# Performance work log

Hardware: AMD Instinct MI355X
Metric: run time of the kernel (lower is better)

The kernel has to match this reference:

```python
import jax, jax.numpy as jnp
import numpy as np

N_EMBD = 768
HIDDEN = 4 * N_EMBD
N_EXPERTS = 8
TOP_K = 2


def setup_inputs() -> dict:
    key = jax.random.key(0)
    ks = jax.random.split(key, 4)
    B, T, C, E, H = 4, 2048, N_EMBD, N_EXPERTS, HIDDEN
    x = jax.random.normal(ks[0], (B, T, C), dtype=jnp.float32)
    gate_w = jax.random.normal(ks[1], (E, C), dtype=jnp.float32) * 0.02
    gate_b = jnp.zeros((E,), dtype=jnp.float32)
    w_fc = jax.random.normal(ks[2], (E, H, C), dtype=jnp.float32) * 0.02
    b_fc = jnp.zeros((E, H), dtype=jnp.float32)
    w_proj = jax.random.normal(ks[3], (E, C, H), dtype=jnp.float32) * 0.02
    b_proj = jnp.zeros((E, C), dtype=jnp.float32)
    return {"x": x, "gate_w": gate_w, "gate_b": gate_b, "w_fc": w_fc,
            "b_fc": b_fc, "w_proj": w_proj, "b_proj": b_proj}


def reference(x, gate_w, gate_b, w_fc, b_fc, w_proj, b_proj):
    B, T, C = x.shape
    E = gate_b.shape[0]
    xf = x.reshape(-1, C)  # [N, C]
    # gating: Linear(C -> E), top-k, softmax over the k selected scores
    scores = xf @ gate_w.T + gate_b                      # [N, E]
    top_s, top_i = jax.lax.top_k(scores, TOP_K)          # [N, K]
    gates = jax.nn.softmax(top_s, axis=-1)               # [N, K]
    # combine weight per (token, expert): sum_k gate[t,k] * 1[top_i[t,k]==e]
    comb = jnp.sum(jax.nn.one_hot(top_i, E, dtype=xf.dtype) * gates[..., None], axis=1)  # [N, E]
    out = jnp.zeros_like(xf)
    for j in range(E):  # loop over fixed small expert count
        h = jax.nn.gelu(xf @ w_fc[j].T + b_fc[j], approximate=True)  # [N, H]
        y = h @ w_proj[j].T + b_proj[j]                              # [N, C]
        out = out + comb[:, j:j + 1] * y
    return out.reshape(B, T, C)
```

## Files before the change

### kernel.cpp

```cpp
#include <hip/hip_runtime.h>
#include <cmath>

#define N_TOK 8192
#define C_DIM 768
#define H_DIM 3072
#define NEXP  8
#define PADCAP 17408
#define MAXMT  136

typedef short short8 __attribute__((ext_vector_type(8)));
typedef float f32x4  __attribute__((ext_vector_type(4)));

__device__ __forceinline__ unsigned short f2b(float f) {
  unsigned int u = __float_as_uint(f);
  u += 0x7fffu + ((u >> 16) & 1u);
  return (unsigned short)(u >> 16);
}
__device__ __forceinline__ float b2f(unsigned short u) {
  return __uint_as_float((unsigned int)u << 16);
}
__device__ __forceinline__ void gll(const char* g, char* l) {
  __builtin_amdgcn_global_load_lds((const __attribute__((address_space(1))) void*)g,
                                   (__attribute__((address_space(3))) void*)l, 16, 0, 0);
}

__global__ __launch_bounds__(256) void gate_kernel(
    const float* __restrict__ x, const float* __restrict__ gw,
    const float* __restrict__ gb, int* __restrict__ counts,
    int* __restrict__ tok_e, int* __restrict__ tok_r, float* __restrict__ tok_w) {
  __shared__ float gwl[NEXP * C_DIM];
  __shared__ double red[256][NEXP];
  int tid = threadIdx.x;
  const float4* gw4 = (const float4*)gw;
  float4* gl4 = (float4*)gwl;
  for (int i = tid; i < NEXP * C_DIM / 4; i += 256) gl4[i] = gw4[i];
  __syncthreads();
  int tl = tid & 63;
  int kc = tid >> 6;
  int t = blockIdx.x * 64 + tl;
  double acc[NEXP];
#pragma unroll
  for (int e = 0; e < NEXP; e++) acc[e] = 0.0;
  const float* xr = x + (size_t)t * C_DIM;
  for (int k = kc * 192; k < kc * 192 + 192; k++) {
    double xv = (double)xr[k];
#pragma unroll
    for (int e = 0; e < NEXP; e++) acc[e] += xv * (double)gwl[e * C_DIM + k];
  }
#pragma unroll
  for (int e = 0; e < NEXP; e++) red[tid][e] = acc[e];
  __syncthreads();
  if (tid < 64) {
    double s[NEXP];
#pragma unroll
    for (int e = 0; e < NEXP; e++)
      s[e] = (double)gb[e] + red[tid][e] + red[tid + 64][e] + red[tid + 128][e] + red[tid + 192][e];
    double best = s[0], sec = -1e300; int bi = 0, si = -1;
#pragma unroll
    for (int e = 1; e < NEXP; e++) {
      if (s[e] > best)      { sec = best; si = bi; best = s[e]; bi = e; }
      else if (s[e] > sec)  { sec = s[e]; si = e; }
    }
    double ex = exp(sec - best);
    double den = 1.0 + ex;
    tok_e[2 * t] = bi;  tok_e[2 * t + 1] = si;
    tok_w[2 * t] = (float)(1.0 / den);  tok_w[2 * t + 1] = (float)(ex / den);
    tok_r[2 * t]     = atomicAdd(&counts[bi], 1);
    tok_r[2 * t + 1] = atomicAdd(&counts[si], 1);
  }
}

__global__ void offsets_kernel(const int* __restrict__ counts, int* __restrict__ po) {
  if (threadIdx.x == 0 && blockIdx.x == 0) {
    int s = 0;
    for (int e = 0; e < NEXP; e++) { po[e] = s; s += (counts[e] + 127) & ~127; }
    po[NEXP] = s;
  }
}

__global__ __launch_bounds__(256) void scatter_kernel(
    const int* __restrict__ tok_e, const int* __restrict__ tok_r,
    const float* __restrict__ tok_w, const int* __restrict__ po,
    int* __restrict__ perm_t, float* __restrict__ perm_w,
    int* __restrict__ tok_pos) {
  int t = blockIdx.x * 256 + threadIdx.x;
#pragma unroll
  for (int k = 0; k < 2; k++) {
    int e = tok_e[2 * t + k];
    int pos = po[e] + tok_r[2 * t + k];
    perm_t[pos] = t;
    perm_w[pos] = tok_w[2 * t + k];
    tok_pos[2 * t + k] = pos;
  }
}

__global__ __launch_bounds__(256) void gather_kernel(
    const float* __restrict__ x, const int* __restrict__ po,
    const int* __restrict__ perm_t, unsigned short* __restrict__ xg) {
  int row = blockIdx.x * 4 + (threadIdx.x >> 6);
  if (row >= po[NEXP]) return;
  int l = threadIdx.x & 63;
  int t = perm_t[row];
  const float4* src = (const float4*)(x + (size_t)t * C_DIM);
  ushort4* dst = (ushort4*)(xg + (size_t)row * C_DIM);
#pragma unroll
  for (int j = 0; j < 3; j++) {
    float4 v = src[l + j * 64];
    ushort4 o; o.x = f2b(v.x); o.y = f2b(v.y); o.z = f2b(v.z); o.w = f2b(v.w);
    dst[l + j * 64] = o;
  }
}

__global__ __launch_bounds__(256) void wconv_kernel(
    const float* __restrict__ wfc, const float* __restrict__ wproj,
    unsigned short* __restrict__ wfcb, unsigned short* __restrict__ wpjb) {
  const int n4 = NEXP * H_DIM * C_DIM / 4;
  int stride = gridDim.x * blockDim.x;
  for (int i = blockIdx.x * blockDim.x + threadIdx.x; i < 2 * n4; i += stride) {
    const float4* s; ushort4* d; int j;
    if (i < n4) { s = (const float4*)wfc;   d = (ushort4*)wfcb; j = i; }
    else        { s = (const float4*)wproj; d = (ushort4*)wpjb; j = i - n4; }
    float4 v = s[j];
    ushort4 o; o.x = f2b(v.x); o.y = f2b(v.y); o.z = f2b(v.z); o.w = f2b(v.w);
    d[j] = o;
  }
}

__device__ __forceinline__ void gemm_core512(
    const unsigned short* A, int lda, const unsigned short* B, int ldb, int K,
    char* lds, int tid, f32x4 acc[4][2]) {
  const int w = tid >> 6, l = tid & 63;
  const int wr = w >> 2, wc = w & 3;
  const int rowa = wr * 64 + (l & 15);
  const int rowb = wc * 32 + (l & 15);
  const int kc = l >> 4;
  const int sa0 = (kc ^ ((rowa >> 1) & 7)) * 16;
  const int sb0 = (kc ^ ((rowb >> 1) & 7)) * 16;
  const int r0 = tid >> 3,          cg0 = (tid & 7) ^ ((r0 >> 1) & 7);
  const int r1 = (512 + tid) >> 3,  cg1 = ((512 + tid) & 7) ^ ((r1 >> 1) & 7);
  const char* gA0 = (const char*)(A + (size_t)r0 * lda) + cg0 * 16;
  const char* gA1 = (const char*)(A + (size_t)r1 * lda) + cg1 * 16;
  const char* gB0 = (const char*)(B + (size_t)r0 * ldb) + cg0 * 16;
  const char* gB1 = (const char*)(B + (size_t)r1 * ldb) + cg1 * 16;
  const int wb = w * 1024;
  const int iters = K >> 6;
  gll(gA0, lds + wb);
  gll(gA1, lds + 8192 + wb);
  gll(gB0, lds + 16384 + wb);
  gll(gB1, lds + 24576 + wb);
#pragma unroll 1
  for (int kt = 0; kt < iters; kt++) {
    __syncthreads();
    if (kt + 1 < iters) {
      size_t kb = (size_t)(kt + 1) * 128;
      char* nb = lds + ((kt + 1) & 1) * 32768;
      gll(gA0 + kb, nb + wb);
      gll(gA1 + kb, nb + 8192 + wb);
      gll(gB0 + kb, nb + 16384 + wb);
      gll(gB1 + kb, nb + 24576 + wb);
    }
    char* bb = lds + (kt & 1) * 32768;
#pragma unroll
    for (int s = 0; s < 2; s++) {
      const int sxa = sa0 ^ (s << 6);
      const int sxb = sb0 ^ (s << 6);
      short8 af[4], bf2[2];
#pragma unroll
      for (int mi = 0; mi < 4; mi++)
        af[mi] = *(const short8*)(bb + (rowa + mi * 16) * 128 + sxa);
#pragma unroll
      for (int ni = 0; ni < 2; ni++)
        bf2[ni] = *(const short8*)(bb + 16384 + (rowb + ni * 16) * 128 + sxb);
#pragma unroll
      for (int mi = 0; mi < 4; mi++)
#pragma unroll
        for (int ni = 0; ni < 2; ni++)
          acc[mi][ni] = __builtin_amdgcn_mfma_f32_16x16x32_bf16(af[mi], bf2[ni], acc[mi][ni], 0, 0, 0);
    }
  }
}

__global__ __launch_bounds__(512, 4) void fc1_kernel(
    const unsigned short* __restrict__ xg, const unsigned short* __restrict__ wfcb,
    const float* __restrict__ bfc, const int* __restrict__ po,
    unsigned short* __restrict__ h) {
  __shared__ char lds[65536];
  int bid = blockIdx.x;
  int r8 = bid & 7, g8 = bid >> 3;
  int col = g8 % 24;
  int Sp  = g8 / 24;
  int y   = r8 * 17 + Sp;
  int row0 = y * 128;
  if (row0 >= po[NEXP]) return;
  int e = 0;
#pragma unroll
  for (int i = 1; i < NEXP; i++) if (row0 >= po[i]) e = i;
  int n0 = col * 128;
  int tid = threadIdx.x;
  f32x4 acc[4][2];
#pragma unroll
  for (int mi = 0; mi < 4; mi++)
#pragma unroll
    for (int ni = 0; ni < 2; ni++) acc[mi][ni] = (f32x4){0.f, 0.f, 0.f, 0.f};
  gemm_core512(xg + (size_t)row0 * C_DIM, C_DIM,
               wfcb + (size_t)e * H_DIM * C_DIM + (size_t)n0 * C_DIM, C_DIM, C_DIM,
               lds, tid, acc);
  int w = tid >> 6, l = tid & 63;
  int wr = w >> 2, wc = w & 3, q = l >> 4;
  const float* bias = bfc + (size_t)e * H_DIM;
#pragma unroll
  for (int ni = 0; ni < 2; ni++) {
    int colw = n0 + wc * 32 + ni * 16 + (l & 15);
    float bv = bias[colw];
#pragma unroll
    for (int mi = 0; mi < 4; mi++) {
#pragma unroll
      for (int r = 0; r < 4; r++) {
        int row = row0 + wr * 64 + mi * 16 + q * 4 + r;
        float v = acc[mi][ni][r] + bv;
        float z = v * fmaf(0.0356774081f, v * v, 0.7978845608f);
        float ex = __builtin_amdgcn_exp2f(-2.8853900818f * z);
        float g = v * __builtin_amdgcn_rcpf(1.0f + ex);
        h[(size_t)row * H_DIM + colw] = f2b(g);
      }
    }
  }
}

__global__ __launch_bounds__(512, 4) void fc2_kernel(
    const unsigned short* __restrict__ h, const unsigned short* __restrict__ wpjb,
    const float* __restrict__ bproj, const int* __restrict__ po,
    const float* __restrict__ perm_w, unsigned short* __restrict__ part) {
  __shared__ char lds[65536];
  int bid = blockIdx.x;
  int r8 = bid & 7, g8 = bid >> 3;
  int col = g8 % 6;
  int Sp  = g8 / 6;
  int S   = r8 * 34 + Sp;
  int z   = S / 136;
  int y   = S - z * 136;
  int row0 = y * 128;
  if (row0 >= po[NEXP]) return;
  int e = 0;
#pragma unroll
  for (int i = 1; i < NEXP; i++) if (row0 >= po[i]) e = i;
  int n0 = col * 128;
  int koff = z * (H_DIM / 2);
  int tid = threadIdx.x;
  f32x4 acc[4][2];
#pragma unroll
  for (int mi = 0; mi < 4; mi++)
#pragma unroll
    for (int ni = 0; ni < 2; ni++) acc[mi][ni] = (f32x4){0.f, 0.f, 0.f, 0.f};
  gemm_core512(h + (size_t)row0 * H_DIM + koff, H_DIM,
               wpjb + (size_t)e * C_DIM * H_DIM + (size_t)n0 * H_DIM + koff, H_DIM, H_DIM / 2,
               lds, tid, acc);
  int w = tid >> 6, l = tid & 63;
  int wr = w >> 2, wc = w & 3, q = l >> 4;
  const float* bias = bproj + (size_t)e * C_DIM;
  unsigned short* pz = part + (size_t)z * PADCAP * C_DIM;
#pragma unroll
  for (int mi = 0; mi < 4; mi++) {
#pragma unroll
    for (int r = 0; r < 4; r++) {
      int pos = row0 + wr * 64 + mi * 16 + q * 4 + r;
      float wgt = perm_w[pos];
#pragma unroll
      for (int ni = 0; ni < 2; ni++) {
        int colw = n0 + wc * 32 + ni * 16 + (l & 15);
        float v = acc[mi][ni][r];
        if (z == 0) v += bias[colw];
        pz[(size_t)pos * C_DIM + colw] = f2b(v * wgt);
      }
    }
  }
}

__global__ __launch_bounds__(256) void combine_kernel(
    const unsigned short* __restrict__ part, const int* __restrict__ tok_pos,
    float* __restrict__ out) {
  const int NC4 = C_DIM / 4;
  int idx = blockIdx.x * 256 + threadIdx.x;
  int t = idx / NC4, c4 = idx - t * NC4;
  int p0 = tok_pos[2 * t], p1 = tok_pos[2 * t + 1];
  const size_t SP = (size_t)PADCAP * C_DIM;
  const unsigned short* r00 = part + (size_t)p0 * C_DIM + c4 * 4;
  const unsigned short* r10 = part + (size_t)p1 * C_DIM + c4 * 4;
  ushort4 v00 = *(const ushort4*)r00;
  ushort4 v01 = *(const ushort4*)(r00 + SP);
  ushort4 v10 = *(const ushort4*)r10;
  ushort4 v11 = *(const ushort4*)(r10 + SP);
  float4 o;
  o.x = b2f(v00.x) + b2f(v01.x) + b2f(v10.x) + b2f(v11.x);
  o.y = b2f(v00.y) + b2f(v01.y) + b2f(v10.y) + b2f(v11.y);
  o.z = b2f(v00.z) + b2f(v01.z) + b2f(v10.z) + b2f(v11.z);
  o.w = b2f(v00.w) + b2f(v01.w) + b2f(v10.w) + b2f(v11.w);
  ((float4*)out)[idx] = o;
}

extern "C" void kernel_launch(void* const* d_in, const int* in_sizes, int n_in,
                              void* d_out, int out_size, void* d_ws, size_t ws_size,
                              hipStream_t stream) {
  const float* x     = (const float*)d_in[0];
  const float* gw    = (const float*)d_in[1];
  const float* gb    = (const float*)d_in[2];
  const float* wfc   = (const float*)d_in[3];
  const float* bfc   = (const float*)d_in[4];
  const float* wproj = (const float*)d_in[5];
  const float* bproj = (const float*)d_in[6];
  float* out = (float*)d_out;
  char* ws = (char*)d_ws;

  int*   counts  = (int*)(ws + 0);
  int*   po      = (int*)(ws + 64);
  int*   tok_e   = (int*)(ws + 256);
  int*   tok_r   = (int*)(ws + 65792);
  float* tok_w   = (float*)(ws + 131328);
  int*   tok_pos = (int*)(ws + 196864);
  int*   perm_t  = (int*)(ws + 262400);
  float* perm_w  = (float*)(ws + 332032);
  const size_t ROUT_END = 401920;
  unsigned short* wpjb = (unsigned short*)(ws + 401920);
  unsigned short* hbuf = (unsigned short*)(ws + 38150656);
  unsigned short* xg   = (unsigned short*)(ws + 145105408);
  unsigned short* wfcb = (unsigned short*)(ws + 171844096);
  unsigned short* part = (unsigned short*)(ws + 145105408);

  hipMemsetAsync(ws, 0, ROUT_END, stream);

  gate_kernel<<<N_TOK / 64, 256, 0, stream>>>(x, gw, gb, counts, tok_e, tok_r, tok_w);
  offsets_kernel<<<1, 64, 0, stream>>>(counts, po);
  scatter_kernel<<<N_TOK / 256, 256, 0, stream>>>(tok_e, tok_r, tok_w, po, perm_t, perm_w, tok_pos);
  gather_kernel<<<PADCAP / 4, 256, 0, stream>>>(x, po, perm_t, xg);
  wconv_kernel<<<2048, 256, 0, stream>>>(wfc, wproj, wfcb, wpjb);
  fc1_kernel<<<8 * 17 * 24, 512, 0, stream>>>(xg, wfcb, bfc, po, hbuf);
  fc2_kernel<<<8 * 34 * 6, 512, 0, stream>>>(hbuf, wpjb, bproj, po, perm_w, part);
  combine_kernel<<<N_TOK * (C_DIM / 4) / 256, 256, 0, stream>>>(part, tok_pos, out);
}
```

Before: 507.5 us.

## Widen GEMM tiles to 128x256 with triple-buffered LDS pipeline

Replaces the 128x128 double-buffered GEMM core with a 128x256 tile using three 48KB LDS stages, prefetching two k-steps ahead and waiting with explicit vmcnt/barrier instead of __syncthreads. Each wave now computes a 64x64 sub-tile (4x4 MFMAs), and s_setprio is raised around the MFMA burst. Grids for fc1 and fc2 are resized to match. The aim is more reuse of A fragments and better hiding of global latency, at the cost of 144KB LDS per block, lower occupancy (2 blocks per CU requested, likely fewer in practice) and more accumulator registers.

Measured after the change: 533.7 us. +5.2%, slower.

```diff
diff --git a/kernel.cpp b/kernel.cpp
--- a/kernel.cpp
+++ b/kernel.cpp
@@ -126,91 +126,106 @@
   }
 }
 
-__device__ __forceinline__ void gemm_core512(
+#define STAGE6(kt, bufbase) do {                                   \
+    size_t kb_ = (size_t)(kt) * 128;                               \
+    char* nb_ = lds + (bufbase);                                   \
+    gll(gA0 + kb_, nb_ + wb);                                      \
+    gll(gA1 + kb_, nb_ + 8192 + wb);                               \
+    gll(gB0p + kb_, nb_ + 16384 + wb);                             \
+    gll(gB1p + kb_, nb_ + 24576 + wb);                             \
+    gll(gB2p + kb_, nb_ + 32768 + wb);                             \
+    gll(gB3p + kb_, nb_ + 40960 + wb);                             \
+  } while (0)
+
+__device__ __forceinline__ void gemm_big(
     const unsigned short* A, int lda, const unsigned short* B, int ldb, int K,
-    char* lds, int tid, f32x4 acc[4][2]) {
+    char* lds, int tid, f32x4 acc[4][4]) {
   const int w = tid >> 6, l = tid & 63;
   const int wr = w >> 2, wc = w & 3;
-  const int rowa = wr * 64 + (l & 15);
-  const int rowb = wc * 32 + (l & 15);
+  const int ra0 = wr * 64 + (l & 15);
+  const int rb0 = wc * 64 + (l & 15);
   const int kc = l >> 4;
-  const int sa0 = (kc ^ ((rowa >> 1) & 7)) * 16;
-  const int sb0 = (kc ^ ((rowb >> 1) & 7)) * 16;
-  const int r0 = tid >> 3,          cg0 = (tid & 7) ^ ((r0 >> 1) & 7);
-  const int r1 = (512 + tid) >> 3,  cg1 = ((512 + tid) & 7) ^ ((r1 >> 1) & 7);
-  const char* gA0 = (const char*)(A + (size_t)r0 * lda) + cg0 * 16;
-  const char* gA1 = (const char*)(A + (size_t)r1 * lda) + cg1 * 16;
-  const char* gB0 = (const char*)(B + (size_t)r0 * ldb) + cg0 * 16;
-  const char* gB1 = (const char*)(B + (size_t)r1 * ldb) + cg1 * 16;
+  const int sa0 = (kc ^ ((ra0 >> 1) & 7)) * 16;
+  const int sb0 = (kc ^ ((rb0 >> 1) & 7)) * 16;
+  const int rA0 = tid >> 3,           cA0 = (tid & 7) ^ ((rA0 >> 1) & 7);
+  const int rA1 = (512 + tid) >> 3,   cA1 = ((512 + tid) & 7) ^ ((rA1 >> 1) & 7);
+  const int rB0 = tid >> 3,           cB0 = (tid & 7) ^ ((rB0 >> 1) & 7);
+  const int rB1 = (512 + tid) >> 3,   cB1 = ((512 + tid) & 7) ^ ((rB1 >> 1) & 7);
+  const int rB2 = (1024 + tid) >> 3,  cB2 = ((1024 + tid) & 7) ^ ((rB2 >> 1) & 7);
+  const int rB3 = (1536 + tid) >> 3,  cB3 = ((1536 + tid) & 7) ^ ((rB3 >> 1) & 7);
+  const char* gA0  = (const char*)(A + (size_t)rA0 * lda) + cA0 * 16;
+  const char* gA1  = (const char*)(A + (size_t)rA1 * lda) + cA1 * 16;
+  const char* gB0p = (const char*)(B + (size_t)rB0 * ldb) + cB0 * 16;
+  const char* gB1p = (const char*)(B + (size_t)rB1 * ldb) + cB1 * 16;
+  const char* gB2p = (const char*)(B + (size_t)rB2 * ldb) + cB2 * 16;
+  const char* gB3p = (const char*)(B + (size_t)rB3 * ldb) + cB3 * 16;
   const int wb = w * 1024;
   const int iters = K >> 6;
-  gll(gA0, lds + wb);
-  gll(gA1, lds + 8192 + wb);
-  gll(gB0, lds + 16384 + wb);
-  gll(gB1, lds + 24576 + wb);
+  STAGE6(0, 0);
+  STAGE6(1, 49152);
+  int bc = 0, bn2 = 98304;
 #pragma unroll 1
   for (int kt = 0; kt < iters; kt++) {
-    __syncthreads();
-    if (kt + 1 < iters) {
-      size_t kb = (size_t)(kt + 1) * 128;
-      char* nb = lds + ((kt + 1) & 1) * 32768;
-      gll(gA0 + kb, nb + wb);
-      gll(gA1 + kb, nb + 8192 + wb);
-      gll(gB0 + kb, nb + 16384 + wb);
-      gll(gB1 + kb, nb + 24576 + wb);
-    }
-    char* bb = lds + (kt & 1) * 32768;
+    if (kt < iters - 1) asm volatile("s_waitcnt vmcnt(6)\n\ts_barrier" ::: "memory");
+    else                asm volatile("s_waitcnt vmcnt(0)\n\ts_barrier" ::: "memory");
+    if (kt + 2 < iters) STAGE6(kt + 2, bn2);
+    char* bb = lds + bc;
 #pragma unroll
     for (int s = 0; s < 2; s++) {
       const int sxa = sa0 ^ (s << 6);
       const int sxb = sb0 ^ (s << 6);
-      short8 af[4], bf2[2];
+      short8 af[4], bf[4];
 #pragma unroll
       for (int mi = 0; mi < 4; mi++)
-        af[mi] = *(const short8*)(bb + (rowa + mi * 16) * 128 + sxa);
-#pragma unroll
-      for (int ni = 0; ni < 2; ni++)
-        bf2[ni] = *(const short8*)(bb + 16384 + (rowb + ni * 16) * 128 + sxb);
+        af[mi] = *(const short8*)(bb + (ra0 + mi * 16) * 128 + sxa);
+#pragma unroll
+      for (int ni = 0; ni < 4; ni++)
+        bf[ni] = *(const short8*)(bb + 16384 + (rb0 + ni * 16) * 128 + sxb);
+      __builtin_amdgcn_s_setprio(1);
 #pragma unroll
       for (int mi = 0; mi < 4; mi++)
 #pragma unroll
-        for (int ni = 0; ni < 2; ni++)
-          acc[mi][ni] = __builtin_amdgcn_mfma_f32_16x16x32_bf16(af[mi], bf2[ni], acc[mi][ni], 0, 0, 0);
+        for (int ni = 0; ni < 4; ni++)
+          acc[mi][ni] = __builtin_amdgcn_mfma_f32_16x16x32_bf16(af[mi], bf[ni], acc[mi][ni], 0, 0, 0);
+      __builtin_amdgcn_s_setprio(0);
+      if (s == 0) asm volatile("s_barrier" ::: "memory");
     }
-  }
-}
-
-__global__ __launch_bounds__(512, 4) void fc1_kernel(
+    bc += 49152;  if (bc == 147456)  bc = 0;
+    bn2 += 49152; if (bn2 == 147456) bn2 = 0;
+  }
+}
+
+__global__ __launch_bounds__(512, 2) void fc1_kernel(
     const unsigned short* __restrict__ xg, const unsigned short* __restrict__ wfcb,
     const float* __restrict__ bfc, const int* __restrict__ po,
     unsigned short* __restrict__ h) {
-  __shared__ char lds[65536];
+  __shared__ char lds[147456];
   int bid = blockIdx.x;
   int r8 = bid & 7, g8 = bid >> 3;
-  int col = g8 % 24;
-  int Sp  = g8 / 24;
+  int col = g8 % 12;
+  int Sp  = g8 / 12;
   int y   = r8 * 17 + Sp;
   int row0 = y * 128;
   if (row0 >= po[NEXP]) return;
   int e = 0;
 #pragma unroll
   for (int i = 1; i < NEXP; i++) if (row0 >= po[i]) e = i;
-  int n0 = col * 128;
+  int n0 = col * 256;
   int tid = threadIdx.x;
-  f32x4 acc[4][2];
+  f32x4 acc[4][4];
 #pragma unroll
   for (int mi = 0; mi < 4; mi++)
 #pragma unroll
-    for (int ni = 0; ni < 2; ni++) acc[mi][ni] = (f32x4){0.f, 0.f, 0.f, 0.f};
-  gemm_core512(xg + (size_t)row0 * C_DIM, C_DIM,
-               wfcb + (size_t)e * H_DIM * C_DIM + (size_t)n0 * C_DIM, C_DIM, C_DIM,
-               lds, tid, acc);
+    for (int ni = 0; ni < 4; ni++) acc[mi][ni] = (f32x4){0.f, 0.f, 0.f, 0.f};
+  gemm_big(xg + (size_t)row0 * C_DIM, C_DIM,
+           wfcb + (size_t)e * H_DIM * C_DIM + (size_t)n0 * C_DIM, C_DIM, C_DIM,
+           lds, tid, acc);
   int w = tid >> 6, l = tid & 63;
   int wr = w >> 2, wc = w & 3, q = l >> 4;
   const float* bias = bfc + (size_t)e * H_DIM;
 #pragma unroll
-  for (int ni = 0; ni < 2; ni++) {
-    int colw = n0 + wc * 32 + ni * 16 + (l & 15);
+  for (int ni = 0; ni < 4; ni++) {
+    int colw = n0 + wc * 64 + ni * 16 + (l & 15);
     float bv = bias[colw];
 #pragma unroll
     for (int mi = 0; mi < 4; mi++) {
@@ -227,34 +242,34 @@
   }
 }
 
-__global__ __launch_bounds__(512, 4) void fc2_kernel(
+__global__ __launch_bounds__(512, 2) void fc2_kernel(
     const unsigned short* __restrict__ h, const unsigned short* __restrict__ wpjb,
     const float* __restrict__ bproj, const int* __restrict__ po,
     const float* __restrict__ perm_w, unsigned short* __restrict__ part) {
-  __shared__ char lds[65536];
+  __shared__ char lds[147456];
   int bid = blockIdx.x;
   int r8 = bid & 7, g8 = bid >> 3;
-  int col = g8 % 6;
-  int Sp  = g8 / 6;
-  int S   = r8 * 34 + Sp;
-  int z   = S / 136;
-  int y   = S - z * 136;
+  int col = g8 % 3;
+  int qq  = g8 / 3;
+  int z   = qq & 1;
+  int Sp  = qq >> 1;
+  int y   = r8 * 17 + Sp;
   int row0 = y * 128;
   if (row0 >= po[NEXP]) return;
   int e = 0;
 #pragma unroll
   for (int i = 1; i < NEXP; i++) if (row0 >= po[i]) e = i;
-  int n0 = col * 128;
+  int n0 = col * 256;
   int koff = z * (H_DIM / 2);
   int tid = threadIdx.x;
-  f32x4 acc[4][2];
+  f32x4 acc[4][4];
 #pragma unroll
   for (int mi = 0; mi < 4; mi++)
 #pragma unroll
-    for (int ni = 0; ni < 2; ni++) acc[mi][ni] = (f32x4){0.f, 0.f, 0.f, 0.f};
-  gemm_core512(h + (size_t)row0 * H_DIM + koff, H_DIM,
-               wpjb + (size_t)e * C_DIM * H_DIM + (size_t)n0 * H_DIM + koff, H_DIM, H_DIM / 2,
-               lds, tid, acc);
+    for (int ni = 0; ni < 4; ni++) acc[mi][ni] = (f32x4){0.f, 0.f, 0.f, 0.f};
+  gemm_big(h + (size_t)row0 * H_DIM + koff, H_DIM,
+           wpjb + (size_t)e * C_DIM * H_DIM + (size_t)n0 * H_DIM + koff, H_DIM, H_DIM / 2,
+           lds, tid, acc);
   int w = tid >> 6, l = tid & 63;
   int wr = w >> 2, wc = w & 3, q = l >> 4;
   const float* bias = bproj + (size_t)e * C_DIM;
@@ -266,8 +281,8 @@
       int pos = row0 + wr * 64 + mi * 16 + q * 4 + r;
       float wgt = perm_w[pos];
 #pragma unroll
-      for (int ni = 0; ni < 2; ni++) {
-        int colw = n0 + wc * 32 + ni * 16 + (l & 15);
+      for (int ni = 0; ni < 4; ni++) {
+        int colw = n0 + wc * 64 + ni * 16 + (l & 15);
         float v = acc[mi][ni][r];
         if (z == 0) v += bias[colw];
         pz[(size_t)pos * C_DIM + colw] = f2b(v * wgt);
@@ -333,7 +348,7 @@
   scatter_kernel<<<N_TOK / 256, 256, 0, stream>>>(tok_e, tok_r, tok_w, po, perm_t, perm_w, tok_pos);
   gather_kernel<<<PADCAP / 4, 256, 0, stream>>>(x, po, perm_t, xg);
   wconv_kernel<<<2048, 256, 0, stream>>>(wfc, wproj, wfcb, wpjb);
-  fc1_kernel<<<8 * 17 * 24, 512, 0, stream>>>(xg, wfcb, bfc, po, hbuf);
-  fc2_kernel<<<8 * 34 * 6, 512, 0, stream>>>(hbuf, wpjb, bproj, po, perm_w, part);
+  fc1_kernel<<<8 * 17 * 12, 512, 0, stream>>>(xg, wfcb, bfc, po, hbuf);
+  fc2_kernel<<<8 * 17 * 3 * 2, 512, 0, stream>>>(hbuf, wpjb, bproj, po, perm_w, part);
   combine_kernel<<<N_TOK * (C_DIM / 4) / 256, 256, 0, stream>>>(part, tok_pos, out);
 }
```
